# Optimization experiments

Measured on AMD Instinct MI355X. Metric: run time of the kernel, lower is better.

The kernel has to match this reference:

```python
import jax, jax.numpy as jnp
import numpy as np

EPS = 1e-10   # module eps added before log_softmax in entropy branch
BETA = 1.0
M, B, C = 4, 8192, 1000


def setup_inputs() -> dict:
    key = jax.random.key(0)
    k1, k2 = jax.random.split(key)
    logits = jax.random.normal(k1, (M, B, C), dtype=jnp.float32)
    targets = jax.random.randint(k2, (B,), 0, C, dtype=jnp.int64)
    return {"logits": logits, "targets": targets}


def reference(logits, targets):
    # logits: (M, B, C) stacked pred_logits_list; targets: (B,)
    m, b, c = logits.shape
    # per-sample cross entropy for each model: (M, B)
    logp = jax.nn.log_softmax(logits, axis=-1)
    ce = -jnp.take_along_axis(logp, targets[None, :, None], axis=2)[..., 0]
    # entropy term: -log(C) - mean(log_softmax(logits + eps)) per sample: (M, B)
    logp_eps = jax.nn.log_softmax(logits + EPS, axis=-1)
    ent = -jnp.log(jnp.float32(c)) - jnp.mean(logp_eps, axis=-1)
    # loss[m] = ce[m] + beta * sum_{j != m} ent[j]
    total_ent = jnp.sum(ent, axis=0)  # (B,)
    loss = ce + BETA * (total_ent[None, :] - ent)  # (M, B)
    # topk=1: per-sample winner model index
    min_index = jnp.argmin(loss, axis=0)  # (B,)
    oracle_logits = logits[min_index, jnp.arange(b)]  # (B, C)
    # scatter mask (M, B): 1 where model m is the winner for sample b
    mask = jax.nn.one_hot(min_index, m, dtype=logits.dtype).T
    new_loss = jnp.sum(mask * (ce - BETA * ent)) / b + BETA * jnp.sum(ent) / b
    return (new_loss, oracle_logits, min_index)
```

## Files before the change

### kernel.cpp

```cpp
#include <hip/hip_runtime.h>
#include <math.h>

#define M_ 4
#define B_ 8192
#define C_ 1000
#define NROWS (M_ * B_)
#define LOGC 6.907755278982137f

__global__ __launch_bounds__(256) void stats_kernel(
    const float* __restrict__ logits, const int* __restrict__ targets,
    float* __restrict__ ce_arr, float* __restrict__ ent_arr) {
  const int wave = threadIdx.x >> 6;
  const int lane = threadIdx.x & 63;
  const int row = blockIdx.x * 4 + wave;
  if (row >= NROWS) return;

  const float* rowp = logits + (size_t)row * C_;
  const float4* p = (const float4*)rowp;

  float4 v[4];
#pragma unroll
  for (int k = 0; k < 4; ++k) {
    int idx = lane + 64 * k;
    if (k < 3 || idx < 250) {
      v[k] = p[idx];
    } else {
      v[k] = make_float4(0.f, 0.f, 0.f, 0.f);
    }
  }
  const int nvalid = (lane < 58) ? 4 : 3;

  float lmax = -INFINITY;
#pragma unroll
  for (int k = 0; k < 4; ++k) {
    if (k < nvalid) {
      lmax = fmaxf(lmax, fmaxf(fmaxf(v[k].x, v[k].y), fmaxf(v[k].z, v[k].w)));
    }
  }
#pragma unroll
  for (int off = 32; off; off >>= 1) lmax = fmaxf(lmax, __shfl_xor(lmax, off));

  float lsum = 0.f, lexp = 0.f;
#pragma unroll
  for (int k = 0; k < 4; ++k) {
    if (k < nvalid) {
      lsum += (v[k].x + v[k].y) + (v[k].z + v[k].w);
      lexp += __expf(v[k].x - lmax) + __expf(v[k].y - lmax) +
              __expf(v[k].z - lmax) + __expf(v[k].w - lmax);
    }
  }
#pragma unroll
  for (int off = 32; off; off >>= 1) {
    lsum += __shfl_xor(lsum, off);
    lexp += __shfl_xor(lexp, off);
  }

  if (lane == 0) {
    const int b = row & (B_ - 1);
    const float lse = lmax + __logf(lexp);
    const float tval = rowp[targets[b]];
    ce_arr[row] = lse - tval;
    ent_arr[row] = lse - lsum * (1.0f / C_) - LOGC;
  }
}

__global__ __launch_bounds__(256) void argmin_kernel(
    const float* __restrict__ ce_arr, const float* __restrict__ ent_arr,
    float* __restrict__ out, int* __restrict__ win_arr) {
  const int b = blockIdx.x * 256 + threadIdx.x;

  float ce[M_], ent[M_], tot = 0.f;
#pragma unroll
  for (int m = 0; m < M_; ++m) {
    ce[m] = ce_arr[m * B_ + b];
    ent[m] = ent_arr[m * B_ + b];
    tot += ent[m];
  }
  float best = ce[0] + (tot - ent[0]);
  int bi = 0;
#pragma unroll
  for (int m = 1; m < M_; ++m) {
    float l = ce[m] + (tot - ent[m]);
    if (l < best) { best = l; bi = m; }
  }
  win_arr[b] = bi;
  out[1 + (size_t)B_ * C_ + b] = (float)bi;

  float contrib = (ce[bi] - ent[bi] + tot) * (1.0f / B_);
#pragma unroll
  for (int off = 32; off; off >>= 1) contrib += __shfl_xor(contrib, off);

  __shared__ float red[4];
  if ((threadIdx.x & 63) == 0) red[threadIdx.x >> 6] = contrib;
  __syncthreads();
  if (threadIdx.x == 0) {
    atomicAdd(out, (red[0] + red[1]) + (red[2] + red[3]));
  }
}

__global__ __launch_bounds__(256) void gather_kernel(
    const float* __restrict__ logits, const int* __restrict__ win_arr,
    float* __restrict__ out) {
  const int b = blockIdx.x;
  const int win = win_arr[b];
  const float* src = logits + ((size_t)win * B_ + b) * C_;
  float* dst = out + 1 + (size_t)b * C_;
  for (int t = threadIdx.x; t < C_; t += 256) dst[t] = src[t];
}

extern "C" void kernel_launch(void* const* d_in, const int* in_sizes, int n_in,
                              void* d_out, int out_size, void* d_ws,
                              size_t ws_size, hipStream_t stream) {
  const float* logits = (const float*)d_in[0];
  const int* targets = (const int*)d_in[1];
  float* out = (float*)d_out;

  float* ce_arr = (float*)d_ws;
  float* ent_arr = ce_arr + NROWS;
  int* win_arr = (int*)(ent_arr + NROWS);

  hipMemsetAsync(d_out, 0, sizeof(float), stream);

  stats_kernel<<<NROWS / 4, 256, 0, stream>>>(logits, targets, ce_arr, ent_arr);
  argmin_kernel<<<B_ / 256, 256, 0, stream>>>(ce_arr, ent_arr, out, win_arr);
  gather_kernel<<<B_, 256, 0, stream>>>(logits, win_arr, out);
}
```

Baseline: 208.6 us.

## Fuse stats, argmin and gather into one kernel per sample

Each block now handles one sample, with its four waves covering the four models. The block computes CE and entropy, picks the winning model through shared memory, and writes the oracle row straight from registers. This removes the re-read of logits in the gather kernel, the ce/ent workspace round-trip, the memset and the atomic. The scalar loss is now computed by a deterministic single-block reduction of per-sample partials. Stores to out+1 are misaligned for float4, so the row is written as scalar stores.

```diff
diff --git a/kernel.cpp b/kernel.cpp
--- a/kernel.cpp
+++ b/kernel.cpp
@@ -4,24 +4,22 @@
 #define M_ 4
 #define B_ 8192
 #define C_ 1000
-#define NROWS (M_ * B_)
 #define LOGC 6.907755278982137f
 
-__global__ __launch_bounds__(256) void stats_kernel(
+__global__ __launch_bounds__(256) void fused_kernel(
     const float* __restrict__ logits, const int* __restrict__ targets,
-    float* __restrict__ ce_arr, float* __restrict__ ent_arr) {
-  const int wave = threadIdx.x >> 6;
+    float* __restrict__ out, float* __restrict__ partials) {
+  const int b = blockIdx.x;
+  const int m = threadIdx.x >> 6;
   const int lane = threadIdx.x & 63;
-  const int row = blockIdx.x * 4 + wave;
-  if (row >= NROWS) return;
 
-  const float* rowp = logits + (size_t)row * C_;
+  const float* rowp = logits + ((size_t)m * B_ + b) * C_;
   const float4* p = (const float4*)rowp;
 
   float4 v[4];
 #pragma unroll
   for (int k = 0; k < 4; ++k) {
-    int idx = lane + 64 * k;
+    const int idx = lane + 64 * k;
     if (k < 3 || idx < 250) {
       v[k] = p[idx];
     } else {
@@ -32,11 +30,9 @@
 
   float lmax = -INFINITY;
 #pragma unroll
-  for (int k = 0; k < 4; ++k) {
-    if (k < nvalid) {
+  for (int k = 0; k < 4; ++k)
+    if (k < nvalid)
       lmax = fmaxf(lmax, fmaxf(fmaxf(v[k].x, v[k].y), fmaxf(v[k].z, v[k].w)));
-    }
-  }
 #pragma unroll
   for (int off = 32; off; off >>= 1) lmax = fmaxf(lmax, __shfl_xor(lmax, off));
 
@@ -55,57 +51,67 @@
     lexp += __shfl_xor(lexp, off);
   }
 
+  __shared__ float s_ce[M_], s_ent[M_];
+  __shared__ int s_win;
   if (lane == 0) {
-    const int b = row & (B_ - 1);
     const float lse = lmax + __logf(lexp);
-    const float tval = rowp[targets[b]];
-    ce_arr[row] = lse - tval;
-    ent_arr[row] = lse - lsum * (1.0f / C_) - LOGC;
+    s_ce[m] = lse - rowp[targets[b]];
+    s_ent[m] = lse - lsum * (1.0f / C_) - LOGC;
+  }
+  __syncthreads();
+
+  if (threadIdx.x == 0) {
+    const float tot = (s_ent[0] + s_ent[1]) + (s_ent[2] + s_ent[3]);
+    float best = s_ce[0] + (tot - s_ent[0]);
+    int bi = 0;
+#pragma unroll
+    for (int j = 1; j < M_; ++j) {
+      const float l = s_ce[j] + (tot - s_ent[j]);
+      if (l < best) { best = l; bi = j; }
+    }
+    s_win = bi;
+    out[1 + (size_t)B_ * C_ + b] = (float)bi;
+    partials[b] = (s_ce[bi] - s_ent[bi] + tot) * (1.0f / B_);
+  }
+  __syncthreads();
+
+  if (m == s_win) {
+    float* dst = out + 1 + (size_t)b * C_;
+#pragma unroll
+    for (int k = 0; k < 4; ++k) {
+      const int idx = lane + 64 * k;
+      if (k < 3 || idx < 250) {
+        const int e = 4 * idx;
+        dst[e + 0] = v[k].x;
+        dst[e + 1] = v[k].y;
+        dst[e + 2] = v[k].z;
+        dst[e + 3] = v[k].w;
+      }
+    }
   }
 }
 
-__global__ __launch_bounds__(256) void argmin_kernel(
-    const float* __restrict__ ce_arr, const float* __restrict__ ent_arr,
-    float* __restrict__ out, int* __restrict__ win_arr) {
-  const int b = blockIdx.x * 256 + threadIdx.x;
+__global__ __launch_bounds__(1024) void reduce_kernel(
+    const float* __restrict__ partials, float* __restrict__ out) {
+  const float4* p4 = (const float4*)partials;
+  float s = 0.f;
+#pragma unroll
+  for (int k = 0; k < 2; ++k) {
+    const float4 v = p4[threadIdx.x + 1024 * k];
+    s += (v.x + v.y) + (v.z + v.w);
+  }
+#pragma unroll
+  for (int off = 32; off; off >>= 1) s += __shfl_xor(s, off);
 
-  float ce[M_], ent[M_], tot = 0.f;
+  __shared__ float red[16];
+  if ((threadIdx.x & 63) == 0) red[threadIdx.x >> 6] = s;
+  __syncthreads();
+  if (threadIdx.x < 16) {
+    float t = red[threadIdx.x];
 #pragma unroll
-  for (int m = 0; m < M_; ++m) {
-    ce[m] = ce_arr[m * B_ + b];
-    ent[m] = ent_arr[m * B_ + b];
-    tot += ent[m];
+    for (int off = 8; off; off >>= 1) t += __shfl_xor(t, off, 16);
+    if (threadIdx.x == 0) out[0] = t;
   }
-  float best = ce[0] + (tot - ent[0]);
-  int bi = 0;
-#pragma unroll
-  for (int m = 1; m < M_; ++m) {
-    float l = ce[m] + (tot - ent[m]);
-    if (l < best) { best = l; bi = m; }
-  }
-  win_arr[b] = bi;
-  out[1 + (size_t)B_ * C_ + b] = (float)bi;
-
-  float contrib = (ce[bi] - ent[bi] + tot) * (1.0f / B_);
-#pragma unroll
-  for (int off = 32; off; off >>= 1) contrib += __shfl_xor(contrib, off);
-
-  __shared__ float red[4];
-  if ((threadIdx.x & 63) == 0) red[threadIdx.x >> 6] = contrib;
-  __syncthreads();
-  if (threadIdx.x == 0) {
-    atomicAdd(out, (red[0] + red[1]) + (red[2] + red[3]));
-  }
-}
-
-__global__ __launch_bounds__(256) void gather_kernel(
-    const float* __restrict__ logits, const int* __restrict__ win_arr,
-    float* __restrict__ out) {
-  const int b = blockIdx.x;
-  const int win = win_arr[b];
-  const float* src = logits + ((size_t)win * B_ + b) * C_;
-  float* dst = out + 1 + (size_t)b * C_;
-  for (int t = threadIdx.x; t < C_; t += 256) dst[t] = src[t];
 }
 
 extern "C" void kernel_launch(void* const* d_in, const int* in_sizes, int n_in,
@@ -114,14 +120,8 @@
   const float* logits = (const float*)d_in[0];
   const int* targets = (const int*)d_in[1];
   float* out = (float*)d_out;
+  float* partials = (float*)d_ws;
 
-  float* ce_arr = (float*)d_ws;
-  float* ent_arr = ce_arr + NROWS;
-  int* win_arr = (int*)(ent_arr + NROWS);
-
-  hipMemsetAsync(d_out, 0, sizeof(float), stream);
-
-  stats_kernel<<<NROWS / 4, 256, 0, stream>>>(logits, targets, ce_arr, ent_arr);
-  argmin_kernel<<<B_ / 256, 256, 0, stream>>>(ce_arr, ent_arr, out, win_arr);
-  gather_kernel<<<B_, 256, 0, stream>>>(logits, win_arr, out);
+  fused_kernel<<<B_, 256, 0, stream>>>(logits, targets, out, partials);
+  reduce_kernel<<<1, 1024, 0, stream>>>(partials, out);
 }
```

Result: faster. 197.7 us (-5.2%).
